# Kernel optimization log

Hardware: AMD Instinct MI355X
Metric: run time of the kernel (lower is better)

Reference implementation:

```python
import jax, jax.numpy as jnp
import numpy as np

CH = (64, 128, 256, 512)
KV = sum(CH)          # 960, kv_size = sum(channel_num)
EPS = 1e-5            # InstanceNorm2d default eps
SCALE = 1.0 / float(np.sqrt(KV))


def setup_inputs() -> dict:
    key = jax.random.key(0)
    ks = jax.random.split(key, 16)
    B, N = 16, 1024
    d = {}
    for i, c in enumerate(CH):
        d[f"emb{i+1}"] = jax.random.normal(ks[i], (B, N, c), jnp.float32)
    d["emb_all"] = jax.random.normal(ks[4], (B, N, KV), jnp.float32)
    for i, c in enumerate(CH):
        # two stacked query heads per branch, Linear weights [out,in]
        d[f"Wq{i+1}"] = jax.random.normal(ks[5 + i], (2, c, c), jnp.float32) * 0.05
        d[f"Wo{i+1}"] = jax.random.normal(ks[9 + i], (c, c), jnp.float32) * 0.05
    d["Wk"] = jax.random.normal(ks[13], (2, KV, KV), jnp.float32) * 0.02
    d["Wv"] = jax.random.normal(ks[14], (2, KV, KV), jnp.float32) * 0.02
    return d


def _attend(emb, Wq, Wo, k, v):
    # emb: [B,N,C]; Wq: [H=2,C,C]; k,v: [B,H,N,KV]
    # torch: stack([Linear(emb) for 2 heads], dim=1).transpose(-1,-2) -> [B,H,C,N]
    q = jnp.einsum('bnc,hdc->bhdn', emb, Wq)
    scores = jnp.einsum('bhdn,bhnk->bhdk', q, k) * SCALE          # [B,H,C,KV]
    # InstanceNorm2d over spatial dims (C,KV) per (batch, head); biased var, no affine
    mu = scores.mean(axis=(2, 3), keepdims=True)
    var = scores.var(axis=(2, 3), keepdims=True)
    probs = jax.nn.softmax((scores - mu) * jax.lax.rsqrt(var + EPS), axis=3)
    # context = probs @ v^T -> [B,H,C,N]; permute(0,3,2,1).mean(3) == mean over heads -> [B,N,C]
    ctx = jnp.einsum('bhdk,bhnk->bnd', probs, v) / probs.shape[1]
    return jnp.einsum('bnd,ed->bne', ctx, Wo)                     # out Linear, no bias


def reference(emb1, emb2, emb3, emb4, emb_all,
              Wq1, Wq2, Wq3, Wq4, Wk, Wv, Wo1, Wo2, Wo3, Wo4):
    # shared multi-head key/value from concatenated embedding: [B,H,N,KV]
    k = jnp.einsum('bnk,hmk->bhnm', emb_all, Wk)
    v = jnp.einsum('bnk,hmk->bhnm', emb_all, Wv)
    outs = [_attend(e, Wq, Wo, k, v) for e, Wq, Wo in (
        (emb1, Wq1, Wo1), (emb2, Wq2, Wo2), (emb3, Wq3, Wo3), (emb4, Wq4, Wo4))]
    # outputs (out1..out4) concatenated along channel for a single array result
    return jnp.concatenate(outs, axis=-1)
```

## Files before the change

kernel.cpp:

```cpp
#include <hip/hip_runtime.h>
#include <cmath>

#define B_   16
#define N_   1024
#define KV_  960
#define H_   2
#define LDP  1024
#define PGE  ((size_t)1024 * 1024)

typedef __attribute__((ext_vector_type(8))) short     short8;
typedef __attribute__((ext_vector_type(8))) unsigned short ushort8;
typedef __attribute__((ext_vector_type(4))) unsigned short ushort4v;
typedef __attribute__((ext_vector_type(4))) float     f32x4;
typedef __attribute__((ext_vector_type(4))) float     float4v;
typedef __attribute__((ext_vector_type(2))) float     float2v;

__device__ inline ushort f2b(float f) {
    union { float f; unsigned u; } x; x.f = f;
    unsigned r = x.u + 0x7FFFu + ((x.u >> 16) & 1u);
    return (ushort)(r >> 16);
}
__device__ inline float b2f(ushort u) {
    union { unsigned u; float f; } x; x.u = (unsigned)u << 16; return x.f;
}

__device__ inline int xcd_swz(int orig, int nwg) {
    int q = nwg >> 3, r = nwg & 7;
    int xcd = orig & 7, idx = orig >> 3;
    return (xcd < r ? xcd * (q + 1) : r * (q + 1) + (xcd - r) * q) + idx;
}

__device__ inline void gload16(const ushort* g, ushort* l) {
    __builtin_amdgcn_global_load_lds(
        (const __attribute__((address_space(1))) void*)g,
        (__attribute__((address_space(3))) void*)l, 16, 0, 0);
}

template<int HSUM, bool OUTF32, bool STATS>
__global__ __launch_bounds__(512)
void gemm256(int gx, int gy, int K, float alpha,
             const ushort* __restrict__ A, size_t sAb, size_t sAh,
             const ushort* __restrict__ Bm, size_t sBb, size_t sBh,
             void* __restrict__ C, int ldc, size_t sCb, size_t sCh, int hsel,
             float2v* __restrict__ parts)
{
    __shared__ ushort As[2][256 * 32];
    __shared__ ushort Bs[2][128 * 32];
    const int wgid = xcd_swz(blockIdx.x, gridDim.x);
    const int xg = wgid % gx, rem = wgid / gx;
    const int yg = rem % gy, z = rem / gy;
    int b, h;
    if (hsel >= 0) { b = z; h = hsel; } else { b = z >> 1; h = z & 1; }
    const int m0 = yg * 256, n0 = xg * 128;
    const int t = threadIdx.x, lane = t & 63, wave = t >> 6;
    const int wr = wave >> 1, wc = wave & 1;

    f32x4 acc[4][4];
#pragma unroll
    for (int i = 0; i < 4; ++i)
#pragma unroll
        for (int j = 0; j < 4; ++j) acc[i][j] = f32x4{0.f, 0.f, 0.f, 0.f};

    int srowA[2], skofA[2];
#pragma unroll
    for (int rep = 0; rep < 2; ++rep) {
        int s = rep * 512 + t;
        srowA[rep] = s >> 2;
        skofA[rep] = ((s & 3) ^ ((srowA[rep] >> 1) & 3)) * 8;
    }
    const int srowB = t >> 2;
    const int skofB = ((t & 3) ^ ((srowB >> 1) & 3)) * 8;

    int aoff[4], boff[4];
#pragma unroll
    for (int i = 0; i < 4; ++i) {
        int ra = wr * 64 + i * 16 + (lane & 15);
        aoff[i] = ra * 32 + (((lane >> 4) ^ ((ra >> 1) & 3)) * 8);
        int rb = wc * 64 + i * 16 + (lane & 15);
        boff[i] = rb * 32 + (((lane >> 4) ^ ((rb >> 1) & 3)) * 8);
    }

    const int ksteps = K >> 5;
    const int total  = HSUM * ksteps;

    auto stage = [&](int s, int buf) {
        const int hh = (HSUM == 2) ? (s >= ksteps ? 1 : 0) : h;
        const int k0 = ((HSUM == 2 && s >= ksteps) ? (s - ksteps) : s) << 5;
        const ushort* Ab = A + (size_t)b * sAb + (size_t)hh * sAh;
        const ushort* Bb = Bm + (size_t)b * sBb + (size_t)hh * sBh;
#pragma unroll
        for (int rep = 0; rep < 2; ++rep)
            gload16(Ab + (size_t)(m0 + srowA[rep]) * LDP + k0 + skofA[rep],
                    &As[buf][(rep * 512 + t) * 8]);
        gload16(Bb + (size_t)(n0 + srowB) * LDP + k0 + skofB, &Bs[buf][t * 8]);
    };

    stage(0, 0);
    __syncthreads();
    int cur = 0;
    for (int s = 0; s < total; ++s) {
        if (s + 1 < total) stage(s + 1, cur ^ 1);
        short8 a[4], bv[4];
#pragma unroll
        for (int i = 0; i < 4; ++i) {
            a[i]  = *(const short8*)&As[cur][aoff[i]];
            bv[i] = *(const short8*)&Bs[cur][boff[i]];
        }
#pragma unroll
        for (int i = 0; i < 4; ++i)
#pragma unroll
            for (int j = 0; j < 4; ++j)
                acc[i][j] = __builtin_amdgcn_mfma_f32_16x16x32_bf16(a[i], bv[j], acc[i][j], 0, 0, 0);
        __syncthreads();
        cur ^= 1;
    }

    char* Cb = (char*)C + ((size_t)b * sCb + (size_t)h * sCh) * (OUTF32 ? 4 : 2);
#pragma unroll
    for (int i = 0; i < 4; ++i) {
        int row = m0 + wr * 64 + i * 16 + (lane >> 4) * 4;
#pragma unroll
        for (int q = 0; q < 4; ++q)
#pragma unroll
            for (int j = 0; j < 4; ++j) {
                int col = n0 + wc * 64 + j * 16 + (lane & 15);
                float v = alpha * acc[i][j][q];
                if (OUTF32) ((float*)Cb)[(size_t)(row + q) * ldc + col] = v;
                else        ((ushort*)Cb)[(size_t)(row + q) * ldc + col] = f2b(v);
            }
    }

    if constexpr (STATS) {
        float s1[4] = {0.f, 0.f, 0.f, 0.f}, s2[4] = {0.f, 0.f, 0.f, 0.f};
#pragma unroll
        for (int i = 0; i < 4; ++i) {
            int row = m0 + wr * 64 + i * 16 + (lane >> 4) * 4;
#pragma unroll
            for (int q = 0; q < 4; ++q) {
                int rr = row + q;
                if (rr >= KV_) continue;
                int br = rr < 64 ? 0 : rr < 192 ? 1 : rr < 448 ? 2 : 3;
#pragma unroll
                for (int j = 0; j < 4; ++j) {
                    int col = n0 + wc * 64 + j * 16 + (lane & 15);
                    if (col >= KV_) continue;
                    float v = alpha * acc[i][j][q];
                    s1[br] += v; s2[br] += v * v;
                }
            }
        }
#pragma unroll
        for (int br = 0; br < 4; ++br)
#pragma unroll
            for (int o = 32; o; o >>= 1) {
                s1[br] += __shfl_down(s1[br], o);
                s2[br] += __shfl_down(s2[br], o);
            }
        __shared__ float red[8][8];
        if (lane == 0) {
#pragma unroll
            for (int br = 0; br < 4; ++br) { red[wave][br] = s1[br]; red[wave][4 + br] = s2[br]; }
        }
        __syncthreads();
        if (t < 4) {
            float S1 = 0.f, S2 = 0.f;
#pragma unroll
            for (int w = 0; w < 8; ++w) { S1 += red[w][t]; S2 += red[w][4 + t]; }
            float2v r; r[0] = S1; r[1] = S2;
            parts[((size_t)z * 32 + yg * 8 + xg) * 4 + t] = r;
        }
    }
}

__device__ inline void stage64b(const ushort* __restrict__ src, int ld, int r0, int k0,
                                ushort* __restrict__ lds, int t)
{
#pragma unroll
    for (int rep = 0; rep < 2; ++rep) {
        int idx = t + rep * 256;
        int rr = idx >> 3, kc = (idx & 7) << 3;
        *(ushort8*)&lds[rr * 72 + kc] =
            *(const ushort8*)(src + (size_t)(r0 + rr) * ld + (k0 + kc));
    }
}

__global__ __launch_bounds__(256)
void ygemm(const ushort* __restrict__ W0, const ushort* __restrict__ W1,
           const ushort* __restrict__ W2, const ushort* __restrict__ W3,
           const ushort* __restrict__ G2, ushort* __restrict__ Y)
{
    __shared__ ushort As[64 * 72];
    __shared__ ushort Bs[64 * 72];
    const int wg = xcd_swz(blockIdx.x, gridDim.x);
    const int z = wg / 225, tl = wg % 225;
    const int b = z >> 1, h = z & 1;
    const int br = tl < 15 ? 0 : tl < 45 ? 1 : tl < 105 ? 2 : 3;
    const int st = br == 0 ? 0 : br == 1 ? 15 : br == 2 ? 45 : 105;
    const int loc = tl - st;
    const int xg = loc % 15, yg = loc / 15;
    const int csz[4]  = {64, 128, 256, 512};
    const int coff[4] = {0, 64, 192, 448};
    const ushort* wp[4] = {W0, W1, W2, W3};
    const int c = csz[br];
    const ushort* A = wp[br] + (size_t)h * c * c;
    const ushort* B = G2 + (size_t)b * PGE + coff[br];
    ushort* Cp = Y + (size_t)b * 2 * PGE + (size_t)h * PGE + (size_t)coff[br] * LDP;
    const int m0 = yg * 64, n0 = xg * 64;
    const int t = threadIdx.x, lane = t & 63, wave = t >> 6;
    const int wr = wave >> 1, wc = wave & 1;

    f32x4 z4 = {0.f, 0.f, 0.f, 0.f};
    f32x4 acc[2][2]; acc[0][0] = z4; acc[0][1] = z4; acc[1][0] = z4; acc[1][1] = z4;

    for (int k0 = 0; k0 < c; k0 += 64) {
        stage64b(A, c, m0, k0, As, t);
        stage64b(B, LDP, n0, k0, Bs, t);
        __syncthreads();
        const int ar = wr * 32 + (lane & 15);
        const int brw = wc * 32 + (lane & 15);
        const int kg = (lane >> 4) * 8;
#pragma unroll
        for (int ks = 0; ks < 2; ++ks) {
            short8 a0 = *(const short8*)&As[(ar)      * 72 + ks * 32 + kg];
            short8 a1 = *(const short8*)&As[(ar + 16) * 72 + ks * 32 + kg];
            short8 b0 = *(const short8*)&Bs[(brw)      * 72 + ks * 32 + kg];
            short8 b1 = *(const short8*)&Bs[(brw + 16) * 72 + ks * 32 + kg];
            acc[0][0] = __builtin_amdgcn_mfma_f32_16x16x32_bf16(a0, b0, acc[0][0], 0, 0, 0);
            acc[0][1] = __builtin_amdgcn_mfma_f32_16x16x32_bf16(a0, b1, acc[0][1], 0, 0, 0);
            acc[1][0] = __builtin_amdgcn_mfma_f32_16x16x32_bf16(a1, b0, acc[1][0], 0, 0, 0);
            acc[1][1] = __builtin_amdgcn_mfma_f32_16x16x32_bf16(a1, b1, acc[1][1], 0, 0, 0);
        }
        __syncthreads();
    }
#pragma unroll
    for (int i = 0; i < 2; ++i)
#pragma unroll
        for (int q = 0; q < 4; ++q) {
            int row = m0 + wr * 32 + i * 16 + (lane >> 4) * 4 + q;
#pragma unroll
            for (int j = 0; j < 2; ++j) {
                int col = n0 + wc * 32 + j * 16 + (lane & 15);
                Cp[(size_t)row * LDP + col] = f2b(acc[i][j][q]);
            }
        }
}

__global__ __launch_bounds__(256)
void ogemm(const ushort* __restrict__ ctx,
           const ushort* __restrict__ O0, const ushort* __restrict__ O1,
           const ushort* __restrict__ O2, const ushort* __restrict__ O3,
           float* __restrict__ out)
{
    __shared__ ushort As[64 * 72];
    __shared__ ushort Bs[64 * 72];
    const int wg = xcd_swz(blockIdx.x, gridDim.x);
    const int b = wg / 240, tl = wg % 240;
    const int br = tl < 16 ? 0 : tl < 48 ? 1 : tl < 112 ? 2 : 3;
    const int st = br == 0 ? 0 : br == 1 ? 16 : br == 2 ? 48 : 112;
    const int loc = tl - st;
    const int csz[4]  = {64, 128, 256, 512};
    const int coff[4] = {0, 64, 192, 448};
    const ushort* op[4] = {O0, O1, O2, O3};
    const int c = csz[br];
    const int gxi = c / 64;
    const int xg = loc % gxi, yg = loc / gxi;
    const ushort* A = ctx + (size_t)b * PGE + coff[br];
    const ushort* B = op[br];
    float* Cf = out + (size_t)b * ((size_t)N_ * KV_) + coff[br];
    const int m0 = yg * 64, n0 = xg * 64;
    const int t = threadIdx.x, lane = t & 63, wave = t >> 6;
    const int wr = wave >> 1, wc = wave & 1;

    f32x4 z4 = {0.f, 0.f, 0.f, 0.f};
    f32x4 acc[2][2]; acc[0][0] = z4; acc[0][1] = z4; acc[1][0] = z4; acc[1][1] = z4;

    for (int k0 = 0; k0 < c; k0 += 64) {
        stage64b(A, LDP, m0, k0, As, t);
        stage64b(B, c, n0, k0, Bs, t);
        __syncthreads();
        const int ar = wr * 32 + (lane & 15);
        const int brw = wc * 32 + (lane & 15);
        const int kg = (lane >> 4) * 8;
#pragma unroll
        for (int ks = 0; ks < 2; ++ks) {
            short8 a0 = *(const short8*)&As[(ar)      * 72 + ks * 32 + kg];
            short8 a1 = *(const short8*)&As[(ar + 16) * 72 + ks * 32 + kg];
            short8 b0 = *(const short8*)&Bs[(brw)      * 72 + ks * 32 + kg];
            short8 b1 = *(const short8*)&Bs[(brw + 16) * 72 + ks * 32 + kg];
            acc[0][0] = __builtin_amdgcn_mfma_f32_16x16x32_bf16(a0, b0, acc[0][0], 0, 0, 0);
            acc[0][1] = __builtin_amdgcn_mfma_f32_16x16x32_bf16(a0, b1, acc[0][1], 0, 0, 0);
            acc[1][0] = __builtin_amdgcn_mfma_f32_16x16x32_bf16(a1, b0, acc[1][0], 0, 0, 0);
            acc[1][1] = __builtin_amdgcn_mfma_f32_16x16x32_bf16(a1, b1, acc[1][1], 0, 0, 0);
        }
        __syncthreads();
    }
#pragma unroll
    for (int i = 0; i < 2; ++i)
#pragma unroll
        for (int q = 0; q < 4; ++q) {
            int row = m0 + wr * 32 + i * 16 + (lane >> 4) * 4 + q;
#pragma unroll
            for (int j = 0; j < 2; ++j) {
                int col = n0 + wc * 32 + j * 16 + (lane & 15);
                Cf[(size_t)row * KV_ + col] = acc[i][j][q];
            }
        }
}

struct WSeg { const float* s; ushort* d; unsigned n; };
struct WcvtA { WSeg seg[8]; };
__global__ __launch_bounds__(256)
void wcvt(WcvtA a)
{
    WSeg sg = a.seg[blockIdx.y];
    for (size_t i = ((size_t)blockIdx.x * 256 + threadIdx.x) * 4; i < sg.n;
         i += (size_t)gridDim.x * 1024) {
        float4v f = *(const float4v*)(sg.s + i);
        ushort4v v;
        v[0] = f2b(f[0]); v[1] = f2b(f[1]); v[2] = f2b(f[2]); v[3] = f2b(f[3]);
        *(ushort4v*)(sg.d + i) = v;
    }
}

__global__ __launch_bounds__(256)
void cvt_ld(const float* __restrict__ src, int sld, size_t sYsrc,
            ushort* __restrict__ dst, int dld, size_t sYdst, int total_chunks)
{
    const float* s0 = src + (size_t)blockIdx.y * sYsrc;
    ushort* d0 = dst + (size_t)blockIdx.y * sYdst;
    for (int ch = blockIdx.x * 256 + threadIdx.x; ch < total_chunks;
         ch += gridDim.x * 256) {
        int row = ch / 120, c = (ch % 120) * 8;
        const float* s = s0 + (size_t)row * sld + c;
        float4v f0 = *(const float4v*)s;
        float4v f1 = *(const float4v*)(s + 4);
        ushort8 v;
        v[0] = f2b(f0[0]); v[1] = f2b(f0[1]); v[2] = f2b(f0[2]); v[3] = f2b(f0[3]);
        v[4] = f2b(f1[0]); v[5] = f2b(f1[1]); v[6] = f2b(f1[2]); v[7] = f2b(f1[3]);
        *(ushort8*)(d0 + (size_t)row * dld + c) = v;
    }
}

__global__ __launch_bounds__(256)
void tposecvt(const float* __restrict__ src, size_t sSrc, int sld,
              ushort* __restrict__ dst, size_t sDst, int dld)
{
    __shared__ ushort tile[32][33];
    const float* s = src + (size_t)blockIdx.z * sSrc;
    ushort* d = dst + (size_t)blockIdx.z * sDst;
    int c0 = blockIdx.x * 32, r0 = blockIdx.y * 32;
    for (int i = threadIdx.y; i < 32; i += 8)
        tile[i][threadIdx.x] = f2b(s[(size_t)(r0 + i) * sld + c0 + threadIdx.x]);
    __syncthreads();
    for (int i = threadIdx.y; i < 32; i += 8)
        d[(size_t)(c0 + i) * dld + r0 + threadIdx.x] = tile[threadIdx.x][i];
}

__global__ __launch_bounds__(256)
void cvtall(const float* __restrict__ ea_src, ushort* __restrict__ ea, size_t sEA,
            ushort* __restrict__ eat, size_t sEAT,
            const float* __restrict__ e0, const float* __restrict__ e1,
            const float* __restrict__ e2, const float* __restrict__ e3,
            ushort* __restrict__ embT)
{
    __shared__ float tile[64][65];
    int tx = threadIdx.x, ty = threadIdx.y;
    if (blockIdx.x < 15) {
        const float* s = ea_src + (size_t)blockIdx.z * ((size_t)N_ * KV_);
        ushort* pea  = ea  + (size_t)blockIdx.z * sEA;
        ushort* peat = eat + (size_t)blockIdx.z * sEAT;
        int m0 = blockIdx.x * 64, n0 = blockIdx.y * 64;
        for (int i = ty; i < 64; i += 4) {
            float v = s[(size_t)(n0 + i) * KV_ + m0 + tx];
            tile[i][tx] = v;
            pea[(size_t)(n0 + i) * LDP + m0 + tx] = f2b(v);
        }
        __syncthreads();
        for (int i = ty; i < 64; i += 4)
            peat[(size_t)(m0 + i) * LDP + n0 + tx] = f2b(tile[tx][i]);
    } else {
        const int xt = blockIdx.x - 15;
        const int br = xt < 1 ? 0 : xt < 3 ? 1 : xt < 7 ? 2 : 3;
        const int st = br == 0 ? 0 : br == 1 ? 1 : br == 2 ? 3 : 7;
        const int loc = xt - st;
        const int csz[4]  = {64, 128, 256, 512};
        const int coff[4] = {0, 64, 192, 448};
        const float* ep[4] = {e0, e1, e2, e3};
        const int c = csz[br];
        const float* s = ep[br] + (size_t)blockIdx.z * ((size_t)N_ * c);
        ushort* d = embT + (size_t)blockIdx.z * (2 * PGE) + (size_t)coff[br] * LDP;
        int c0 = loc * 64, r0 = blockIdx.y * 64;
        for (int i = ty; i < 64; i += 4)
            tile[i][tx] = s[(size_t)(r0 + i) * c + c0 + tx];
        __syncthreads();
        for (int i = ty; i < 64; i += 4)
            d[(size_t)(c0 + i) * LDP + r0 + tx] = f2b(tile[tx][i]);
    }
}

__global__ __launch_bounds__(64)
void normstats2b(const float2v* __restrict__ parts, float* __restrict__ stats)
{
    const int z = blockIdx.x;
    const int bh = z >> 2, br = z & 3;
    const int csz[4] = {64, 128, 256, 512};
    if (threadIdx.x == 0) {
        float s = 0.f, s2 = 0.f;
        const float2v* p = parts + (size_t)bh * 128 + br;
        for (int t = 0; t < 32; ++t) {
            float2v r = p[t * 4];
            s += r[0]; s2 += r[1];
        }
        const float inv_cnt = 1.0f / (float)(csz[br] * KV_);
        float mu  = s * inv_cnt;
        float var = s2 * inv_cnt - mu * mu;
        stats[2 * z]     = mu;
        stats[2 * z + 1] = rsqrtf(var + 1e-5f);
    }
}

__global__ __launch_bounds__(256)
void psoftmax(ushort* __restrict__ S, const float* __restrict__ stats)
{
    const int r  = blockIdx.x;
    const int bh  = r / KV_;
    const int row = r % KV_;
    const int br  = (row < 64) ? 0 : (row < 192) ? 1 : (row < 448) ? 2 : 3;
    const float mu = stats[2 * (bh * 4 + br)];
    const float rs = stats[2 * (bh * 4 + br) + 1];
    ushort* p = S + (size_t)bh * PGE + (size_t)row * LDP;

    const int t = threadIdx.x;
    float x[4];
    float s = 0.f;
#pragma unroll
    for (int i = 0; i < 4; ++i) {
        int idx = t + i * 256;
        x[i] = (idx < KV_) ? __expf((b2f(p[idx]) - mu) * rs) : 0.f;
        s += x[i];
    }
#pragma unroll
    for (int o = 1; o < 64; o <<= 1) s += __shfl_xor(s, o);
    __shared__ float wsum[4];
    int w = t >> 6, l = t & 63;
    if (l == 0) wsum[w] = s;
    __syncthreads();
    s = wsum[0] + wsum[1] + wsum[2] + wsum[3];
    float inv = 1.0f / s;
#pragma unroll
    for (int i = 0; i < 4; ++i) {
        int idx = t + i * 256;
        if (idx < KV_) p[idx] = f2b(x[i] * inv);
    }
}

extern "C" void kernel_launch(void* const* d_in, const int* in_sizes, int n_in,
                              void* d_out, int out_size, void* d_ws, size_t ws_size,
                              hipStream_t stream)
{
    const float* emb[4] = {(const float*)d_in[0], (const float*)d_in[1],
                           (const float*)d_in[2], (const float*)d_in[3]};
    const float* emb_all = (const float*)d_in[4];
    const float* Wq[4] = {(const float*)d_in[5], (const float*)d_in[7],
                          (const float*)d_in[9], (const float*)d_in[11]};
    const float* Wo[4] = {(const float*)d_in[6], (const float*)d_in[8],
                          (const float*)d_in[10], (const float*)d_in[12]};
    const float* Wk = (const float*)d_in[13];
    const float* Wv = (const float*)d_in[14];
    float* out = (float*)d_out;

    const int c_sz[4]  = {64, 128, 256, 512};

    const size_t BN  = (size_t)N_ * KV_;
    const size_t GE9 = (size_t)KV_ * KV_;
    const float SCALE = 0.03227486121839514f;

    char* wsp = (char*)d_ws;
    size_t off = 0;
    auto alloc = [&](size_t bytes) -> char* {
        off = (off + 255) & ~(size_t)255;
        char* p = wsp + off;
        off += bytes;
        return p;
    };

    ushort* WqB[4]; ushort* WoB[4];
    for (int i = 0; i < 4; ++i) WqB[i] = (ushort*)alloc((size_t)2 * c_sz[i] * c_sz[i] * 2);
    for (int i = 0; i < 4; ++i) WoB[i] = (ushort*)alloc((size_t)c_sz[i] * c_sz[i] * 2);
    ushort* WkB = (ushort*)alloc(2 * PGE * 2);
    ushort* WvT = (ushort*)alloc(2 * PGE * 2);

    {
        WcvtA a;
        for (int i = 0; i < 4; ++i) {
            a.seg[i]     = { Wq[i], WqB[i], (unsigned)(2 * c_sz[i] * c_sz[i]) };
            a.seg[4 + i] = { Wo[i], WoB[i], (unsigned)(c_sz[i] * c_sz[i]) };
        }
        wcvt<<<dim3(64, 8), 256, 0, stream>>>(a);
    }
    cvt_ld<<<dim3(450, 2), 256, 0, stream>>>(Wk, KV_, GE9, WkB, LDP, PGE, 960 * 120);
    tposecvt<<<dim3(30, 30, 2), dim3(32, 8), 0, stream>>>(Wv, GE9, KV_, WvT, PGE, LDP);

    const size_t perB = 6 * PGE * 2;
    size_t statik = (off + 255) & ~(size_t)255;
    int NB = 16;
    while (NB > 1 && statik + (size_t)NB * perB + 262144 > ws_size) NB >>= 1;

    ushort* slotA = (ushort*)alloc((size_t)NB * PGE * 2);
    ushort* Y     = (ushort*)alloc((size_t)NB * 2 * PGE * 2);
    ushort* Sc    = (ushort*)alloc((size_t)NB * 2 * PGE * 2);
    ushort* EA    = (ushort*)alloc((size_t)NB * PGE * 2);
    float*  stats = (float*) alloc((size_t)NB * 2 * 4 * 2 * 4);
    float2v* parts = (float2v*)alloc((size_t)NB * 2 * 64 * 4 * 8);
    ushort* EAT  = Sc;
    ushort* embT = Y;
    ushort* R    = Y;

    for (int b0 = 0; b0 < B_; b0 += NB) {
        cvtall<<<dim3(30, 16, NB), dim3(64, 4), 0, stream>>>(
            emb_all + (size_t)b0 * BN, EA, PGE, EAT, 2 * PGE,
            emb[0] + (size_t)b0 * N_ * 64,  emb[1] + (size_t)b0 * N_ * 128,
            emb[2] + (size_t)b0 * N_ * 256, emb[3] + (size_t)b0 * N_ * 512,
            embT);

        gemm256<1, false, false><<<dim3(8 * 4 * NB), 512, 0, stream>>>(
            8, 4, N_, 1.0f,
            EAT, 2 * PGE, 0,
            embT, 2 * PGE, 0,
            slotA, LDP, PGE, 0, 0, nullptr);

        ygemm<<<dim3(NB * 2 * 225), 256, 0, stream>>>(
            WqB[0], WqB[1], WqB[2], WqB[3], slotA, Y);

        gemm256<1, false, true><<<dim3(8 * 4 * NB * H_), 512, 0, stream>>>(
            8, 4, KV_, SCALE,
            Y, 2 * PGE, PGE,
            WkB, 0, PGE,
            Sc, LDP, 2 * PGE, PGE, -1, parts);

        normstats2b<<<NB * H_ * 4, 64, 0, stream>>>(parts, stats);
        psoftmax<<<NB * H_ * KV_, 256, 0, stream>>>(Sc, stats);

        gemm256<2, false, false><<<dim3(8 * 4 * NB), 512, 0, stream>>>(
            8, 4, KV_, 1.0f,
            Sc, 2 * PGE, PGE,
            WvT, 0, PGE,
            R, LDP, 2 * PGE, 0, 0, nullptr);

        gemm256<1, false, false><<<dim3(8 * 4 * NB), 512, 0, stream>>>(
            8, 4, KV_, 0.5f,
            EA, PGE, 0,
            R, 2 * PGE, 0,
            slotA, LDP, PGE, 0, 0, nullptr);

        ogemm<<<dim3(NB * 240), 256, 0, stream>>>(
            slotA, WoB[0], WoB[1], WoB[2], WoB[3],
            out + (size_t)b0 * BN);
    }
}
```

Measured before the change: 434.1 us.

## Triple-buffer LDS in gemm256 with prefetch depth two and vmcnt waits

Switches the main GEMM's shared-memory staging from double to triple buffering, issuing global-to-LDS loads two k-steps ahead. It replaces __syncthreads with an explicit s_waitcnt vmcnt plus s_barrier, so loads for the next stage can stay in flight while the current stage computes. The cost is 50% more LDS per block (72KB), which may lower occupancy. A barrier is added before the stats reduction because the final iteration no longer syncs.

Result: slower. 626.2 us (+44.3%).

```diff
diff --git a/kernel.cpp b/kernel.cpp
--- a/kernel.cpp
+++ b/kernel.cpp
@@ -44,8 +44,8 @@
              void* __restrict__ C, int ldc, size_t sCb, size_t sCh, int hsel,
              float2v* __restrict__ parts)
 {
-    __shared__ ushort As[2][256 * 32];
-    __shared__ ushort Bs[2][128 * 32];
+    __shared__ ushort AsF[3 * 256 * 32];
+    __shared__ ushort BsF[3 * 128 * 32];
     const int wgid = xcd_swz(blockIdx.x, gridDim.x);
     const int xg = wgid % gx, rem = wgid / gx;
     const int yg = rem % gy, z = rem / gy;
@@ -88,31 +88,50 @@
         const int k0 = ((HSUM == 2 && s >= ksteps) ? (s - ksteps) : s) << 5;
         const ushort* Ab = A + (size_t)b * sAb + (size_t)hh * sAh;
         const ushort* Bb = Bm + (size_t)b * sBb + (size_t)hh * sBh;
+        const int aB = buf * (256 * 32), bB = buf * (128 * 32);
 #pragma unroll
         for (int rep = 0; rep < 2; ++rep)
             gload16(Ab + (size_t)(m0 + srowA[rep]) * LDP + k0 + skofA[rep],
-                    &As[buf][(rep * 512 + t) * 8]);
-        gload16(Bb + (size_t)(n0 + srowB) * LDP + k0 + skofB, &Bs[buf][t * 8]);
+                    &AsF[aB + (rep * 512 + t) * 8]);
+        gload16(Bb + (size_t)(n0 + srowB) * LDP + k0 + skofB, &BsF[bB + t * 8]);
     };
 
+    auto compute = [&](int buf) {
+        const int aB = buf * (256 * 32), bB = buf * (128 * 32);
+        short8 a[4], bv[4];
+#pragma unroll
+        for (int i = 0; i < 4; ++i) {
+            a[i]  = *(const short8*)&AsF[aB + aoff[i]];
+            bv[i] = *(const short8*)&BsF[bB + boff[i]];
+        }
+#pragma unroll
+        for (int i = 0; i < 4; ++i)
+#pragma unroll
+            for (int j = 0; j < 4; ++j)
+                acc[i][j] = __builtin_amdgcn_mfma_f32_16x16x32_bf16(a[i], bv[j], acc[i][j], 0, 0, 0);
+    };
+
     stage(0, 0);
-    __syncthreads();
+    stage(1, 1);
+    asm volatile("s_waitcnt vmcnt(3)" ::: "memory");
+    __builtin_amdgcn_s_barrier();
+
     int cur = 0;
     for (int s = 0; s < total; ++s) {
-        if (s + 1 < total) stage(s + 1, cur ^ 1);
-        short8 a[4], bv[4];
-#pragma unroll
-        for (int i = 0; i < 4; ++i) {
-            a[i]  = *(const short8*)&As[cur][aoff[i]];
-            bv[i] = *(const short8*)&Bs[cur][boff[i]];
-        }
-#pragma unroll
-        for (int i = 0; i < 4; ++i)
-#pragma unroll
-            for (int j = 0; j < 4; ++j)
-                acc[i][j] = __builtin_amdgcn_mfma_f32_16x16x32_bf16(a[i], bv[j], acc[i][j], 0, 0, 0);
-        __syncthreads();
-        cur ^= 1;
+        if (s + 2 < total) {
+            int tgt = cur + 2; if (tgt >= 3) tgt -= 3;
+            stage(s + 2, tgt);
+            compute(cur);
+            asm volatile("s_waitcnt vmcnt(3)" ::: "memory");
+            __builtin_amdgcn_s_barrier();
+        } else {
+            compute(cur);
+            if (s + 1 < total) {
+                asm volatile("s_waitcnt vmcnt(0)" ::: "memory");
+                __builtin_amdgcn_s_barrier();
+            }
+        }
+        cur = cur + 1; if (cur >= 3) cur -= 3;
     }
 
     char* Cb = (char*)C + ((size_t)b * sCb + (size_t)h * sCh) * (OUTF32 ? 4 : 2);
@@ -157,6 +176,7 @@
                 s2[br] += __shfl_down(s2[br], o);
             }
         __shared__ float red[8][8];
+        __syncthreads();
         if (lane == 0) {
 #pragma unroll
             for (int br = 0; br < 4; ++br) { red[wave][br] = s1[br]; red[wave][4 + br] = s2[br]; }
```
